# Optimization experiments

Measured on AMD Instinct MI355X. Metric: run time of the kernel, lower is better.

The kernel has to match this reference:

```python
import jax, jax.numpy as jnp
import numpy as np

SEQ, BATCH, HIDDEN = 2048, 1, 4096
NUM_HEADS, NUM_KV_HEADS, HEAD_DIM = 32, 8, 128
Q_PER_GROUP = NUM_HEADS // NUM_KV_HEADS  # 4
TOTAL_PROJ = NUM_KV_HEADS * (Q_PER_GROUP + 2) * HEAD_DIM  # 6144


def setup_inputs() -> dict:
    key = jax.random.key(0)
    k1, k2, k3 = jax.random.split(key, 3)
    tokens = jax.random.normal(k1, (SEQ, BATCH, HIDDEN), dtype=jnp.float32)
    # xavier-ish scaling so activations stay sane
    weight_qkv = jax.random.normal(k2, (TOTAL_PROJ, HIDDEN), dtype=jnp.float32) * (2.0 / (TOTAL_PROJ + HIDDEN)) ** 0.5
    weight_proj = jax.random.normal(k3, (HIDDEN, NUM_HEADS * HEAD_DIM), dtype=jnp.float32) * (2.0 / (HIDDEN + NUM_HEADS * HEAD_DIM)) ** 0.5
    return {"tokens": tokens, "weight_qkv": weight_qkv, "weight_proj": weight_proj}


def reference(tokens, weight_qkv, weight_proj):
    S, B, H = tokens.shape
    scale = 1.0 / HEAD_DIM ** 0.5
    # QKV projection with interleaved GQA layout: per KV group [q0..q_{g-1}, k, v]
    qkv = jnp.einsum('sbh,ph->sbp', tokens, weight_qkv)
    qkv = qkv.reshape(S, B, NUM_KV_HEADS, Q_PER_GROUP + 2, HEAD_DIM)
    q = qkv[:, :, :, :Q_PER_GROUP, :].reshape(S, B, NUM_HEADS, HEAD_DIM)
    k = qkv[:, :, :, Q_PER_GROUP, :]       # [S,B,KVH,D]
    v = qkv[:, :, :, Q_PER_GROUP + 1, :]
    # repeat_interleave KV heads to match Q heads (GQA)
    k = jnp.repeat(k, Q_PER_GROUP, axis=2)
    v = jnp.repeat(v, Q_PER_GROUP, axis=2)
    # [S,B,H,D] -> [B,H,S,D]
    q = q.transpose(1, 2, 0, 3)
    k = k.transpose(1, 2, 0, 3)
    v = v.transpose(1, 2, 0, 3)
    scores = jnp.einsum('bhsd,bhtd->bhst', q, k) * scale
    causal = jnp.tril(jnp.ones((S, S), dtype=bool))
    scores = jnp.where(causal, scores, jnp.finfo(scores.dtype).min)
    attn = jax.nn.softmax(scores, axis=-1)
    out = jnp.einsum('bhst,bhtd->bhsd', attn, v)
    # [B,H,S,D] -> [S,B,H*D]
    out = out.transpose(2, 0, 1, 3).reshape(S, B, NUM_HEADS * HEAD_DIM)
    return jnp.einsum('sbe,he->sbh', out, weight_proj)
```

## Files before the change

kernel.cpp:

```cpp
#include <hip/hip_runtime.h>
#include <hip/hip_bf16.h>
#include <stdint.h>

#define SEQ 2048
#define HIDDEN 4096
#define NHEADS 32
#define HD 128
#define QKV_LD 6144
#define OUT_LD 4096

typedef __attribute__((ext_vector_type(8))) short short8;
typedef __attribute__((ext_vector_type(4))) short short4v;
typedef __attribute__((ext_vector_type(4))) float f32x4;
typedef __attribute__((ext_vector_type(4))) int int4v;
typedef __attribute__((ext_vector_type(2))) unsigned int uint2v;
typedef __attribute__((ext_vector_type(4))) float float4v;

__device__ __forceinline__ short f2bf(float f) {
  uint32_t u = __builtin_bit_cast(uint32_t, f);
  u += 0x7fff + ((u >> 16) & 1);
  return (short)(u >> 16);
}

__global__ void cast_kernel(const float* __restrict__ in, short* __restrict__ out, int n4) {
  int stride = gridDim.x * blockDim.x;
  for (int i = blockIdx.x * blockDim.x + threadIdx.x; i < n4; i += stride) {
    float4v v = ((const float4v*)in)[i];
    short4v o;
    o[0] = f2bf(v[0]); o[1] = f2bf(v[1]); o[2] = f2bf(v[2]); o[3] = f2bf(v[3]);
    ((short4v*)out)[i] = o;
  }
}

template <typename OT, int NBF>
__global__ __launch_bounds__(512, 2) void gemm256b(const short* __restrict__ A,
                                                   const short* __restrict__ B,
                                                   OT* __restrict__ C,
                                                   int M, int N, int K, int NT) {
  __shared__ __align__(16) short lds[32768 + NBF * 8192];
  const int tid = threadIdx.x;
  const int w = tid >> 6, lane = tid & 63;
  const int wr = w >> 2, wc = w & 3;
  const int llo = lane & 15, lhi = lane >> 4;

  const int xcd = (int)blockIdx.x & 7;
  const int i = (int)blockIdx.x >> 3;
  const int nt = xcd * (NT >> 3) + (i >> 3);
  const int mt = i & 7;
  const size_t arow0 = (size_t)mt * 256, brow0 = (size_t)nt * (NBF * 64);
  const short* Ab = A + arow0 * K;
  const short* Bb = B + brow0 * K;

  f32x4 acc[8][NBF] = {};

  auto STAGE_A = [&](int kt, int j) {
    const int bufd = kt & 1;
    const int r0 = (j << 6) + (w << 3);
    const int row = r0 + (lane >> 3);
    const short* src = Ab + (size_t)row * K + (kt << 6) + (((lane & 7) ^ (row & 7)) << 3);
    short* dst = lds + (bufd << 14) + r0 * 64;
    __builtin_amdgcn_global_load_lds(
        (const __attribute__((address_space(1))) uint32_t*)src,
        (__attribute__((address_space(3))) uint32_t*)dst, 16, 0, 0);
  };
  auto STAGE_B = [&](int kt, int j) {
    const int bufd = kt & 1;
    const int r0 = (j << 6) + (w << 3);
    const int row = r0 + (lane >> 3);
    const short* src = Bb + (size_t)row * K + (kt << 6) + (((lane & 7) ^ (row & 7)) << 3);
    short* dst = lds + 32768 + bufd * (NBF << 12) + r0 * 64;
    __builtin_amdgcn_global_load_lds(
        (const __attribute__((address_space(1))) uint32_t*)src,
        (__attribute__((address_space(3))) uint32_t*)dst, 16, 0, 0);
  };
  auto STAGE = [&](int kt) {
#pragma unroll
    for (int j = 0; j < 4; j++) STAGE_A(kt, j);
#pragma unroll
    for (int j = 0; j < NBF; j++) STAGE_B(kt, j);
  };

  auto LDA = [&](int bufd, int m, int kk) -> short8 {
    const int row = (wr << 7) + (m << 4) + llo;
    const int ch = ((kk << 2) + lhi) ^ (row & 7);
    return *(const short8*)(lds + (bufd << 14) + row * 64 + (ch << 3));
  };
  auto LDB = [&](int bufd, int n, int kk) -> short8 {
    const int row = wc * (NBF << 4) + (n << 4) + llo;
    const int ch = ((kk << 2) + lhi) ^ (row & 7);
    return *(const short8*)(lds + 32768 + bufd * (NBF << 12) + row * 64 + (ch << 3));
  };

  STAGE(0);
  STAGE(1);
  if constexpr (NBF == 3) asm volatile("s_waitcnt vmcnt(7)" ::: "memory");
  else                    asm volatile("s_waitcnt vmcnt(6)" ::: "memory");
  __builtin_amdgcn_s_barrier();

  const int NKT = K >> 6;
  for (int kt = 0; kt < NKT; ++kt) {
    const int bufd = kt & 1;
    short8 b_[NBF][2];
#pragma unroll
    for (int n = 0; n < NBF; n++) { b_[n][0] = LDB(bufd, n, 0); b_[n][1] = LDB(bufd, n, 1); }
#pragma unroll
    for (int m = 0; m < 8; m++) {
      short8 a0 = LDA(bufd, m, 0);
      short8 a1 = LDA(bufd, m, 1);
#pragma unroll
      for (int n = 0; n < NBF; n++) {
        acc[m][n] = __builtin_amdgcn_mfma_f32_16x16x32_bf16(a0, b_[n][0], acc[m][n], 0, 0, 0);
        acc[m][n] = __builtin_amdgcn_mfma_f32_16x16x32_bf16(a1, b_[n][1], acc[m][n], 0, 0, 0);
      }
    }
    asm volatile("s_waitcnt lgkmcnt(0)" ::: "memory");
    __builtin_amdgcn_s_barrier();
    if (kt + 2 < NKT) STAGE(kt + 2);
    if (kt + 1 < NKT) {
      if (kt + 2 < NKT) {
        if constexpr (NBF == 3) asm volatile("s_waitcnt vmcnt(7)" ::: "memory");
        else                    asm volatile("s_waitcnt vmcnt(6)" ::: "memory");
      } else {
        asm volatile("s_waitcnt vmcnt(0)" ::: "memory");
      }
      __builtin_amdgcn_s_barrier();
    }
  }

#pragma unroll
  for (int m = 0; m < 8; m++)
#pragma unroll
    for (int n = 0; n < NBF; n++)
#pragma unroll
      for (int r = 0; r < 4; r++) {
        const size_t row = arow0 + (wr << 7) + (m << 4) + (lhi << 2) + r;
        const size_t col = brow0 + wc * (NBF << 4) + (n << 4) + llo;
        const float v = acc[m][n][r];
        if constexpr (sizeof(OT) == 2) C[row * N + col] = f2bf(v);
        else                           C[row * N + col] = v;
      }
}

__global__ __launch_bounds__(512) void attn_fwd(const short* __restrict__ qkv,
                                                short* __restrict__ aout) {
  const int qt = gridDim.y - 1 - blockIdx.y;
  const int h = blockIdx.x;
  const int kvh = h >> 2, g = h & 3;
  const int tid = threadIdx.x;
  const int wave = tid >> 6, lane = tid & 63;
  const int lhi = lane >> 4, llo = lane & 15;

  __shared__ __align__(16) short Ksm[2][64 * 128];
  __shared__ __align__(16) short Vsm[2][64 * 128];
  __shared__ __align__(16) short Psm[8][16 * 72];

  const float scale2 = 0.08838834764831845f * 1.4426950408889634f;

  const int qrow = qt * 128 + wave * 16 + llo;
  const short* qbase = qkv + (size_t)qrow * QKV_LD + (kvh * 6 + g) * HD;
  short8 qf[4];
#pragma unroll
  for (int kk = 0; kk < 4; kk++) qf[kk] = *(const short8*)(qbase + kk * 32 + lhi * 8);

  f32x4 o[8] = {};
  float mrow[4], lrow[4];
#pragma unroll
  for (int r = 0; r < 4; r++) { mrow[r] = -1e30f; lrow[r] = 0.f; }

  const short* Kg = qkv + (kvh * 6 + 4) * HD;
  const short* Vg = qkv + (kvh * 6 + 5) * HD;

  auto STAGE_K = [&](int t, int buf) {
#pragma unroll
    for (int c = 0; c < 2; c++) {
      const int call = wave * 2 + c;
      const int row = call * 4 + lhi;
      const int sc = llo ^ (row & 7);
      __builtin_amdgcn_global_load_lds(
          (const __attribute__((address_space(1))) uint32_t*)(Kg + (size_t)(t * 64 + row) * QKV_LD + sc * 8),
          (__attribute__((address_space(3))) uint32_t*)(&Ksm[buf][0] + call * 512), 16, 0, 0);
    }
  };
  short8 vreg[2];
  auto LOAD_V = [&](int t) {
#pragma unroll
    for (int c = 0; c < 2; c++) {
      const int idx = c * 512 + tid;
      const int vr = idx >> 4;
      vreg[c] = *(const short8*)(Vg + (size_t)(t * 64 + vr) * QKV_LD + (idx & 15) * 8);
    }
  };
  auto WRITE_V = [&](int buf) {
#pragma unroll
    for (int c = 0; c < 2; c++) {
      const int idx = c * 512 + tid;
      const int vr = idx >> 4, vc = idx & 15;
      *(short8*)(&Vsm[buf][0] + ((vr >> 2) * 8 + (vc >> 1)) * 64 + (vr & 3) * 16 + (vc & 1) * 8) = vreg[c];
    }
  };

  const uint32_t vlane0 = (uint32_t)(uintptr_t)(__attribute__((address_space(3))) short*)(&Vsm[0][0])
                          + (uint32_t)(lhi * 2048 + llo * 8);

  STAGE_K(0, 0);
  LOAD_V(0);
  asm volatile("s_waitcnt vmcnt(0)" ::: "memory");
  WRITE_V(0);
  __syncthreads();

  const int ntiles = 2 * qt + 2;
  const int qpos0 = qt * 128 + wave * 16 + lhi * 4;
  for (int t = 0; t < ntiles; t++) {
    const int cur = t & 1, nxt = cur ^ 1;
    const bool pf = (t + 1 < ntiles);
    if (pf) { STAGE_K(t + 1, nxt); LOAD_V(t + 1); }

    const short* Kc = &Ksm[cur][0];
    f32x4 s[4] = {};
#pragma unroll
    for (int n = 0; n < 4; n++) {
#pragma unroll
      for (int kk = 0; kk < 4; kk++) {
        const int krow = n * 16 + llo;
        const int ch = (kk * 4 + lhi) ^ (krow & 7);
        short8 kf = *(const short8*)(Kc + krow * 128 + ch * 8);
        s[n] = __builtin_amdgcn_mfma_f32_16x16x32_bf16(qf[kk], kf, s[n], 0, 0, 0);
      }
    }

    float sv[4][4];
    if (t >= 2 * qt) {
#pragma unroll
      for (int n = 0; n < 4; n++)
#pragma unroll
        for (int r = 0; r < 4; r++) {
          float x = s[n][r] * scale2;
          if (t * 64 + n * 16 + llo > qpos0 + r) x = -1e30f;
          sv[n][r] = x;
        }
    } else {
#pragma unroll
      for (int n = 0; n < 4; n++)
#pragma unroll
        for (int r = 0; r < 4; r++) sv[n][r] = s[n][r] * scale2;
    }

    float rm4[4];
#pragma unroll
    for (int r = 0; r < 4; r++) {
      float rm = fmaxf(fmaxf(sv[0][r], sv[1][r]), fmaxf(sv[2][r], sv[3][r]));
#pragma unroll
      for (int msk = 1; msk < 16; msk <<= 1) rm = fmaxf(rm, __shfl_xor(rm, msk));
      rm4[r] = rm;
    }
    bool need = false;
#pragma unroll
    for (int r = 0; r < 4; r++) need = need || (rm4[r] > mrow[r] + 8.0f);
    if (__any(need)) {
#pragma unroll
      for (int r = 0; r < 4; r++) {
        const float mnew = fmaxf(mrow[r], rm4[r]);
        const float a = exp2f(mrow[r] - mnew);
        mrow[r] = mnew;
        lrow[r] *= a;
#pragma unroll
        for (int nn = 0; nn < 8; nn++) o[nn][r] *= a;
      }
    }
#pragma unroll
    for (int r = 0; r < 4; r++) {
      float rs = 0.f;
#pragma unroll
      for (int n = 0; n < 4; n++) {
        float p = exp2f(sv[n][r] - mrow[r]);
        sv[n][r] = p;
        rs += p;
      }
#pragma unroll
      for (int msk = 1; msk < 16; msk <<= 1) rs += __shfl_xor(rs, msk);
      lrow[r] += rs;
    }

    short* P = &Psm[wave][0];
#pragma unroll
    for (int n = 0; n < 4; n++)
#pragma unroll
      for (int r = 0; r < 4; r++)
        P[(lhi * 4 + r) * 72 + n * 16 + llo] = f2bf(sv[n][r]);

    short8 pa0 = *(const short8*)(P + llo * 72 + lhi * 8);
    short8 pa1 = *(const short8*)(P + llo * 72 + 32 + lhi * 8);
    const uint32_t vbase = vlane0 + (uint32_t)(cur * 16384);
#pragma unroll
    for (int ks = 0; ks < 2; ks++) {
      uint2v vr_[8][2];
#pragma unroll
      for (int nn = 0; nn < 8; nn++)
#pragma unroll
        for (int hh = 0; hh < 2; hh++) {
          asm volatile("ds_read_b64_tr_b16 %0, %1 offset:%2"
                       : "=v"(vr_[nn][hh])
                       : "v"(vbase), "i"(ks * 8192 + hh * 1024 + nn * 128));
        }
      asm volatile("s_waitcnt lgkmcnt(0)" ::: "memory");
      __builtin_amdgcn_sched_barrier(0);
      const short8 pa = ks ? pa1 : pa0;
#pragma unroll
      for (int nn = 0; nn < 8; nn++) {
        int4v tv;
        tv[0] = (int)vr_[nn][0][0]; tv[1] = (int)vr_[nn][0][1];
        tv[2] = (int)vr_[nn][1][0]; tv[3] = (int)vr_[nn][1][1];
        o[nn] = __builtin_amdgcn_mfma_f32_16x16x32_bf16(pa, __builtin_bit_cast(short8, tv), o[nn], 0, 0, 0);
      }
    }

    if (pf) {
      asm volatile("s_waitcnt vmcnt(0)" ::: "memory");
      __syncthreads();
      WRITE_V(nxt);
      __syncthreads();
    }
  }

#pragma unroll
  for (int nn = 0; nn < 8; nn++)
#pragma unroll
    for (int r = 0; r < 4; r++) {
      const size_t row = qt * 128 + wave * 16 + lhi * 4 + r;
      const size_t col = (size_t)h * HD + nn * 16 + llo;
      aout[row * OUT_LD + col] = f2bf(o[nn][r] / lrow[r]);
    }
}

extern "C" void kernel_launch(void* const* d_in, const int* in_sizes, int n_in,
                              void* d_out, int out_size, void* d_ws, size_t ws_size,
                              hipStream_t stream) {
  const float* tokens = (const float*)d_in[0];
  const float* wqkv   = (const float*)d_in[1];
  const float* wproj  = (const float*)d_in[2];
  float* out = (float*)d_out;

  short* tok_bf   = (short*)d_ws;
  short* wqkv_bf  = tok_bf   + (size_t)SEQ * HIDDEN;
  short* wproj_bf = wqkv_bf  + (size_t)QKV_LD * HIDDEN;
  short* qkv_bf   = wproj_bf + (size_t)HIDDEN * OUT_LD;
  short* attn_bf  = qkv_bf   + (size_t)SEQ * QKV_LD;

  cast_kernel<<<2048, 256, 0, stream>>>(tokens, tok_bf, SEQ * HIDDEN / 4);
  cast_kernel<<<2048, 256, 0, stream>>>(wqkv, wqkv_bf, QKV_LD * HIDDEN / 4);
  cast_kernel<<<2048, 256, 0, stream>>>(wproj, wproj_bf, HIDDEN * OUT_LD / 4);

  gemm256b<short, 3><<<256, 512, 0, stream>>>(tok_bf, wqkv_bf, qkv_bf, SEQ, QKV_LD, HIDDEN, QKV_LD / 192);

  attn_fwd<<<dim3(NHEADS, SEQ / 128), 512, 0, stream>>>(qkv_bf, attn_bf);

  gemm256b<float, 2><<<256, 512, 0, stream>>>(attn_bf, wproj_bf, out, SEQ, OUT_LD, HIDDEN, OUT_LD / 128);
}
```

Baseline: 316.7 us.

## Fuse fp32-to-bf16 weight casting into GEMM B-operand staging

Drops the two separate weight cast kernels and makes both GEMMs read the fp32 weights directly. The B tiles are now loaded into registers, converted to bf16, and written swizzled into LDS, while A keeps its direct global-to-LDS path. This saves writing and re-reading bf16 weight copies plus two kernel launches. In exchange, B global traffic inside the GEMMs doubles, staging spends VGPRs and VALU cycles, and the pipeline waits on vmcnt counts more tightly, which could lower occupancy or add stalls.

Result: slower. 332.3 us (+4.9%).

```diff
diff --git a/kernel.cpp b/kernel.cpp
--- a/kernel.cpp
+++ b/kernel.cpp
@@ -34,7 +34,7 @@
 
 template <typename OT, int NBF>
 __global__ __launch_bounds__(512, 2) void gemm256b(const short* __restrict__ A,
-                                                   const short* __restrict__ B,
+                                                   const float* __restrict__ B,
                                                    OT* __restrict__ C,
                                                    int M, int N, int K, int NT) {
   __shared__ __align__(16) short lds[32768 + NBF * 8192];
@@ -49,35 +49,44 @@
   const int mt = i & 7;
   const size_t arow0 = (size_t)mt * 256, brow0 = (size_t)nt * (NBF * 64);
   const short* Ab = A + arow0 * K;
-  const short* Bb = B + brow0 * K;
+  const float* Bb = B + brow0 * K;
 
   f32x4 acc[8][NBF] = {};
+
+  const int s_r = lane >> 3;
+  const int s_c = lane & 7;
 
   auto STAGE_A = [&](int kt, int j) {
     const int bufd = kt & 1;
     const int r0 = (j << 6) + (w << 3);
-    const int row = r0 + (lane >> 3);
-    const short* src = Ab + (size_t)row * K + (kt << 6) + (((lane & 7) ^ (row & 7)) << 3);
+    const int row = r0 + s_r;
+    const short* src = Ab + (size_t)row * K + (kt << 6) + ((s_c ^ (row & 7)) << 3);
     short* dst = lds + (bufd << 14) + r0 * 64;
     __builtin_amdgcn_global_load_lds(
         (const __attribute__((address_space(1))) uint32_t*)src,
         (__attribute__((address_space(3))) uint32_t*)dst, 16, 0, 0);
   };
-  auto STAGE_B = [&](int kt, int j) {
+
+  float4v breg[NBF][2];
+  auto LOAD_B = [&](int kt) {
+#pragma unroll
+    for (int j = 0; j < NBF; j++) {
+      const int row = (j << 6) + (w << 3) + s_r;
+      const float* src = Bb + (size_t)row * K + (kt << 6) + (s_c << 3);
+      breg[j][0] = *(const float4v*)src;
+      breg[j][1] = *(const float4v*)(src + 4);
+    }
+  };
+  auto WRITE_B = [&](int kt) {
     const int bufd = kt & 1;
-    const int r0 = (j << 6) + (w << 3);
-    const int row = r0 + (lane >> 3);
-    const short* src = Bb + (size_t)row * K + (kt << 6) + (((lane & 7) ^ (row & 7)) << 3);
-    short* dst = lds + 32768 + bufd * (NBF << 12) + r0 * 64;
-    __builtin_amdgcn_global_load_lds(
-        (const __attribute__((address_space(1))) uint32_t*)src,
-        (__attribute__((address_space(3))) uint32_t*)dst, 16, 0, 0);
-  };
-  auto STAGE = [&](int kt) {
-#pragma unroll
-    for (int j = 0; j < 4; j++) STAGE_A(kt, j);
-#pragma unroll
-    for (int j = 0; j < NBF; j++) STAGE_B(kt, j);
+#pragma unroll
+    for (int j = 0; j < NBF; j++) {
+      const int row = (j << 6) + (w << 3) + s_r;
+      short8 v;
+#pragma unroll
+      for (int e = 0; e < 4; e++) { v[e] = f2bf(breg[j][0][e]); v[4 + e] = f2bf(breg[j][1][e]); }
+      *(short8*)(lds + 32768 + bufd * (NBF << 12) + row * 64 + ((s_c ^ (row & 7)) << 3)) = v;
+    }
   };
 
   auto LDA = [&](int bufd, int m, int kk) -> short8 {
@@ -91,15 +100,22 @@
     return *(const short8*)(lds + 32768 + bufd * (NBF << 12) + row * 64 + (ch << 3));
   };
 
-  STAGE(0);
-  STAGE(1);
-  if constexpr (NBF == 3) asm volatile("s_waitcnt vmcnt(7)" ::: "memory");
-  else                    asm volatile("s_waitcnt vmcnt(6)" ::: "memory");
+  const int NKT = K >> 6;
+
+  LOAD_B(0);
+  WRITE_B(0);
+  LOAD_B(1);
+  WRITE_B(1);
+#pragma unroll
+  for (int j = 0; j < 4; j++) STAGE_A(0, j);
+#pragma unroll
+  for (int j = 0; j < 4; j++) STAGE_A(1, j);
+  asm volatile("s_waitcnt vmcnt(4) lgkmcnt(0)" ::: "memory");
   __builtin_amdgcn_s_barrier();
 
-  const int NKT = K >> 6;
   for (int kt = 0; kt < NKT; ++kt) {
     const int bufd = kt & 1;
+    if (kt + 2 < NKT) LOAD_B(kt + 2);
     short8 b_[NBF][2];
 #pragma unroll
     for (int n = 0; n < NBF; n++) { b_[n][0] = LDB(bufd, n, 0); b_[n][1] = LDB(bufd, n, 1); }
@@ -115,14 +131,15 @@
     }
     asm volatile("s_waitcnt lgkmcnt(0)" ::: "memory");
     __builtin_amdgcn_s_barrier();
-    if (kt + 2 < NKT) STAGE(kt + 2);
-    if (kt + 1 < NKT) {
-      if (kt + 2 < NKT) {
-        if constexpr (NBF == 3) asm volatile("s_waitcnt vmcnt(7)" ::: "memory");
-        else                    asm volatile("s_waitcnt vmcnt(6)" ::: "memory");
-      } else {
-        asm volatile("s_waitcnt vmcnt(0)" ::: "memory");
-      }
+    if (kt + 2 < NKT) {
+#pragma unroll
+      for (int j = 0; j < 4; j++) STAGE_A(kt + 2, j);
+      asm volatile("s_waitcnt vmcnt(4)" ::: "memory");
+      WRITE_B(kt + 2);
+      asm volatile("s_waitcnt lgkmcnt(0)" ::: "memory");
+      __builtin_amdgcn_s_barrier();
+    } else if (kt + 1 < NKT) {
+      asm volatile("s_waitcnt vmcnt(0)" ::: "memory");
       __builtin_amdgcn_s_barrier();
     }
   }
@@ -340,19 +357,15 @@
   const float* wproj  = (const float*)d_in[2];
   float* out = (float*)d_out;
 
-  short* tok_bf   = (short*)d_ws;
-  short* wqkv_bf  = tok_bf   + (size_t)SEQ * HIDDEN;
-  short* wproj_bf = wqkv_bf  + (size_t)QKV_LD * HIDDEN;
-  short* qkv_bf   = wproj_bf + (size_t)HIDDEN * OUT_LD;
-  short* attn_bf  = qkv_bf   + (size_t)SEQ * QKV_LD;
+  short* tok_bf  = (short*)d_ws;
+  short* qkv_bf  = tok_bf  + (size_t)SEQ * HIDDEN;
+  short* attn_bf = qkv_bf  + (size_t)SEQ * QKV_LD;
 
   cast_kernel<<<2048, 256, 0, stream>>>(tokens, tok_bf, SEQ * HIDDEN / 4);
-  cast_kernel<<<2048, 256, 0, stream>>>(wqkv, wqkv_bf, QKV_LD * HIDDEN / 4);
-  cast_kernel<<<2048, 256, 0, stream>>>(wproj, wproj_bf, HIDDEN * OUT_LD / 4);
-
-  gemm256b<short, 3><<<256, 512, 0, stream>>>(tok_bf, wqkv_bf, qkv_bf, SEQ, QKV_LD, HIDDEN, QKV_LD / 192);
+
+  gemm256b<short, 3><<<256, 512, 0, stream>>>(tok_bf, wqkv, qkv_bf, SEQ, QKV_LD, HIDDEN, QKV_LD / 192);
 
   attn_fwd<<<dim3(NHEADS, SEQ / 128), 512, 0, stream>>>(qkv_bf, attn_bf);
 
-  gemm256b<float, 2><<<256, 512, 0, stream>>>(attn_bf, wproj_bf, out, SEQ, OUT_LD, HIDDEN, OUT_LD / 128);
-}
+  gemm256b<float, 2><<<256, 512, 0, stream>>>(attn_bf, wproj, out, SEQ, OUT_LD, HIDDEN, OUT_LD / 128);
+}
```

## Enlarge attention KV tile to 128 and single-buffer V in LDS

Applied to the files above, without the earlier changes.

The attention KV tile grows from 64 to 128 rows, which halves the loop trip count and the per-tile softmax and shuffle overhead. K stays double-buffered through global_load_lds. V is now single-buffered: it is loaded at the start of each iteration and written to LDS between two barriers after the P computation. V load latency is therefore only partly hidden behind QK^T, and LDS use and register pressure rise with the larger tile.

Measured after the change: 304.0 us. -4.0%, faster.

```diff
diff --git a/kernel.cpp b/kernel.cpp
--- a/kernel.cpp
+++ b/kernel.cpp
@@ -150,9 +150,9 @@
   const int wave = tid >> 6, lane = tid & 63;
   const int lhi = lane >> 4, llo = lane & 15;
 
-  __shared__ __align__(16) short Ksm[2][64 * 128];
-  __shared__ __align__(16) short Vsm[2][64 * 128];
-  __shared__ __align__(16) short Psm[8][16 * 72];
+  __shared__ __align__(16) short Ksm[2][128 * 128];
+  __shared__ __align__(16) short Vsm[128 * 128];
+  __shared__ __align__(16) short Psm[8][16 * 136];
 
   const float scale2 = 0.08838834764831845f * 1.4426950408889634f;
 
@@ -172,53 +172,50 @@
 
   auto STAGE_K = [&](int t, int buf) {
 #pragma unroll
-    for (int c = 0; c < 2; c++) {
-      const int call = wave * 2 + c;
+    for (int c = 0; c < 4; c++) {
+      const int call = wave * 4 + c;
       const int row = call * 4 + lhi;
       const int sc = llo ^ (row & 7);
       __builtin_amdgcn_global_load_lds(
-          (const __attribute__((address_space(1))) uint32_t*)(Kg + (size_t)(t * 64 + row) * QKV_LD + sc * 8),
+          (const __attribute__((address_space(1))) uint32_t*)(Kg + (size_t)(t * 128 + row) * QKV_LD + sc * 8),
           (__attribute__((address_space(3))) uint32_t*)(&Ksm[buf][0] + call * 512), 16, 0, 0);
     }
   };
-  short8 vreg[2];
+  short8 vreg[4];
   auto LOAD_V = [&](int t) {
 #pragma unroll
-    for (int c = 0; c < 2; c++) {
+    for (int c = 0; c < 4; c++) {
       const int idx = c * 512 + tid;
       const int vr = idx >> 4;
-      vreg[c] = *(const short8*)(Vg + (size_t)(t * 64 + vr) * QKV_LD + (idx & 15) * 8);
-    }
-  };
-  auto WRITE_V = [&](int buf) {
-#pragma unroll
-    for (int c = 0; c < 2; c++) {
+      vreg[c] = *(const short8*)(Vg + (size_t)(t * 128 + vr) * QKV_LD + (idx & 15) * 8);
+    }
+  };
+  auto WRITE_V = [&]() {
+#pragma unroll
+    for (int c = 0; c < 4; c++) {
       const int idx = c * 512 + tid;
       const int vr = idx >> 4, vc = idx & 15;
-      *(short8*)(&Vsm[buf][0] + ((vr >> 2) * 8 + (vc >> 1)) * 64 + (vr & 3) * 16 + (vc & 1) * 8) = vreg[c];
-    }
-  };
-
-  const uint32_t vlane0 = (uint32_t)(uintptr_t)(__attribute__((address_space(3))) short*)(&Vsm[0][0])
+      *(short8*)(&Vsm[0] + ((vr >> 2) * 8 + (vc >> 1)) * 64 + (vr & 3) * 16 + (vc & 1) * 8) = vreg[c];
+    }
+  };
+
+  const uint32_t vlane0 = (uint32_t)(uintptr_t)(__attribute__((address_space(3))) short*)(&Vsm[0])
                           + (uint32_t)(lhi * 2048 + llo * 8);
 
   STAGE_K(0, 0);
-  LOAD_V(0);
-  asm volatile("s_waitcnt vmcnt(0)" ::: "memory");
-  WRITE_V(0);
   __syncthreads();
 
-  const int ntiles = 2 * qt + 2;
+  const int ntiles = qt + 1;
   const int qpos0 = qt * 128 + wave * 16 + lhi * 4;
   for (int t = 0; t < ntiles; t++) {
     const int cur = t & 1, nxt = cur ^ 1;
-    const bool pf = (t + 1 < ntiles);
-    if (pf) { STAGE_K(t + 1, nxt); LOAD_V(t + 1); }
+    LOAD_V(t);
+    if (t + 1 < ntiles) STAGE_K(t + 1, nxt);
 
     const short* Kc = &Ksm[cur][0];
-    f32x4 s[4] = {};
-#pragma unroll
-    for (int n = 0; n < 4; n++) {
+    f32x4 s[8] = {};
+#pragma unroll
+    for (int n = 0; n < 8; n++) {
 #pragma unroll
       for (int kk = 0; kk < 4; kk++) {
         const int krow = n * 16 + llo;
@@ -228,19 +225,19 @@
       }
     }
 
-    float sv[4][4];
-    if (t >= 2 * qt) {
-#pragma unroll
-      for (int n = 0; n < 4; n++)
+    float sv[8][4];
+    if (t == qt) {
+#pragma unroll
+      for (int n = 0; n < 8; n++)
 #pragma unroll
         for (int r = 0; r < 4; r++) {
           float x = s[n][r] * scale2;
-          if (t * 64 + n * 16 + llo > qpos0 + r) x = -1e30f;
+          if (t * 128 + n * 16 + llo > qpos0 + r) x = -1e30f;
           sv[n][r] = x;
         }
     } else {
 #pragma unroll
-      for (int n = 0; n < 4; n++)
+      for (int n = 0; n < 8; n++)
 #pragma unroll
         for (int r = 0; r < 4; r++) sv[n][r] = s[n][r] * scale2;
     }
@@ -248,7 +245,9 @@
     float rm4[4];
 #pragma unroll
     for (int r = 0; r < 4; r++) {
-      float rm = fmaxf(fmaxf(sv[0][r], sv[1][r]), fmaxf(sv[2][r], sv[3][r]));
+      float rm = sv[0][r];
+#pragma unroll
+      for (int n = 1; n < 8; n++) rm = fmaxf(rm, sv[n][r]);
 #pragma unroll
       for (int msk = 1; msk < 16; msk <<= 1) rm = fmaxf(rm, __shfl_xor(rm, msk));
       rm4[r] = rm;
@@ -271,7 +270,7 @@
     for (int r = 0; r < 4; r++) {
       float rs = 0.f;
 #pragma unroll
-      for (int n = 0; n < 4; n++) {
+      for (int n = 0; n < 8; n++) {
         float p = exp2f(sv[n][r] - mrow[r]);
         sv[n][r] = p;
         rs += p;
@@ -283,16 +282,21 @@
 
     short* P = &Psm[wave][0];
 #pragma unroll
-    for (int n = 0; n < 4; n++)
+    for (int n = 0; n < 8; n++)
 #pragma unroll
       for (int r = 0; r < 4; r++)
-        P[(lhi * 4 + r) * 72 + n * 16 + llo] = f2bf(sv[n][r]);
-
-    short8 pa0 = *(const short8*)(P + llo * 72 + lhi * 8);
-    short8 pa1 = *(const short8*)(P + llo * 72 + 32 + lhi * 8);
-    const uint32_t vbase = vlane0 + (uint32_t)(cur * 16384);
-#pragma unroll
-    for (int ks = 0; ks < 2; ks++) {
+        P[(lhi * 4 + r) * 136 + n * 16 + llo] = f2bf(sv[n][r]);
+    short8 pa[4];
+#pragma unroll
+    for (int ks = 0; ks < 4; ks++)
+      pa[ks] = *(const short8*)(P + llo * 136 + ks * 32 + lhi * 8);
+
+    __syncthreads();
+    WRITE_V();
+    __syncthreads();
+
+#pragma unroll
+    for (int ks = 0; ks < 4; ks++) {
       uint2v vr_[8][2];
 #pragma unroll
       for (int nn = 0; nn < 8; nn++)
@@ -300,25 +304,17 @@
         for (int hh = 0; hh < 2; hh++) {
           asm volatile("ds_read_b64_tr_b16 %0, %1 offset:%2"
                        : "=v"(vr_[nn][hh])
-                       : "v"(vbase), "i"(ks * 8192 + hh * 1024 + nn * 128));
+                       : "v"(vlane0), "i"(ks * 8192 + hh * 1024 + nn * 128));
         }
       asm volatile("s_waitcnt lgkmcnt(0)" ::: "memory");
       __builtin_amdgcn_sched_barrier(0);
-      const short8 pa = ks ? pa1 : pa0;
 #pragma unroll
       for (int nn = 0; nn < 8; nn++) {
         int4v tv;
         tv[0] = (int)vr_[nn][0][0]; tv[1] = (int)vr_[nn][0][1];
         tv[2] = (int)vr_[nn][1][0]; tv[3] = (int)vr_[nn][1][1];
-        o[nn] = __builtin_amdgcn_mfma_f32_16x16x32_bf16(pa, __builtin_bit_cast(short8, tv), o[nn], 0, 0, 0);
-      }
-    }
-
-    if (pf) {
-      asm volatile("s_waitcnt vmcnt(0)" ::: "memory");
-      __syncthreads();
-      WRITE_V(nxt);
-      __syncthreads();
+        o[nn] = __builtin_amdgcn_mfma_f32_16x16x32_bf16(pa[ks], __builtin_bit_cast(short8, tv), o[nn], 0, 0, 0);
+      }
     }
   }
 
```
